# Kernel tuning notes

Measured on AMD Instinct MI355X. Metric: run time of the kernel, lower is better.

The kernel has to match this reference:

```python
import jax, jax.numpy as jnp
import numpy as np


def setup_inputs() -> dict:
    key = jax.random.key(0)
    k1, k2, k3 = jax.random.split(key, 3)
    B, T, D, U = 64, 1024, 256, 256
    inputs = jax.random.normal(k1, (B, T, D), dtype=jnp.float32)
    W_xh = jax.random.normal(k2, (D, U), dtype=jnp.float32) * (1.0 / np.sqrt(D))
    W_hh = jax.random.normal(k3, (U, U), dtype=jnp.float32) * (1.0 / np.sqrt(U))
    b_h = jnp.zeros((U,), dtype=jnp.float32)
    return {"inputs": inputs, "W_xh": W_xh, "W_hh": W_hh, "b_h": b_h}


def reference(inputs, W_xh, W_hh, b_h):
    # inputs: [B, T, D]. Precompute input projection (same math as per-step matmul),
    # then scan the sequential recurrence: h_t = tanh(xW_t + h_{t-1} @ W_hh + b).
    B = inputs.shape[0]
    U = W_hh.shape[0]
    xW = jnp.einsum('btd,du->btu', inputs, W_xh) + b_h  # [B, T, U]
    h0 = jnp.zeros((B, U), dtype=inputs.dtype)

    def step(h, xw_t):
        h_new = jnp.tanh(xw_t + h @ W_hh)
        return h_new, h_new

    _, hs = jax.lax.scan(step, h0, jnp.swapaxes(xW, 0, 1))  # hs: [T, B, U]
    return jnp.swapaxes(hs, 0, 1)  # [B, T, U] (return_sequences=True)
```

## Files before the change

kernel.cpp:

```cpp
#include <hip/hip_runtime.h>
#include <math.h>

#define B_ 64
#define T_ 1024
#define D_ 256
#define U_ 256

typedef __fp16   hf2_t __attribute__((ext_vector_type(2)));
typedef _Float16 f16x8 __attribute__((ext_vector_type(8)));
typedef float    f32x4 __attribute__((ext_vector_type(4)));

__device__ __forceinline__ float fast_tanh2(float x) {
    float e = __expf(2.0f * x);
    return 1.0f - 2.0f * __builtin_amdgcn_rcpf(e + 1.0f);
}

#define CH_  16
#define NCH_ (T_ / CH_)
#define NT2_ 512

__global__ __launch_bounds__(NT2_) __attribute__((amdgpu_waves_per_eu(2, 2)))
void rnn_fused(const float* __restrict__ inputs,
               const float* __restrict__ W_xh,
               const float* __restrict__ W_hh,
               const float* __restrict__ b_h,
               float* __restrict__ out) {
    const int b    = (int)blockIdx.x;
    const int tid  = (int)threadIdx.x;
    const int w    = tid >> 6;
    const int lane = tid & 63;
    const int g    = lane >> 4;
    const int c    = lane & 15;
    const int n0   = w * 32;
    const int cp   = n0 + 2 * c;

    __shared__ __align__(16) _Float16 hl[2][U_];
    __shared__ __align__(16) _Float16 Ax[CH_ * D_];

    f16x8 whh[8][2], wxh[8][2];
    #pragma unroll
    for (int kt = 0; kt < 8; ++kt) {
        #pragma unroll
        for (int nt = 0; nt < 2; ++nt) {
            f16x8 vh, vx;
            #pragma unroll
            for (int j = 0; j < 8; ++j) {
                const int row = kt * 32 + g * 8 + j;
                vh[j] = (_Float16)W_hh[(size_t)row * U_ + cp + nt];
                vx[j] = (_Float16)W_xh[(size_t)row * U_ + cp + nt];
            }
            whh[kt][nt] = vh;
            wxh[kt][nt] = vx;
        }
    }
    const float bb0 = b_h[cp];
    const float bb1 = b_h[cp + 1];

    if (tid < 128) ((float*)&hl[0][0])[tid] = 0.f;

    const float* ibase = inputs + (size_t)b * T_ * D_;
    float* gbase = out + (size_t)b * T_ * U_;

    const int srow = tid >> 5;
    const int sk8  = (tid & 31) * 8;
    char* const sdst = (char*)Ax + srow * 512 + ((sk8 * 2) ^ ((srow & 7) << 4));
    const int vbaseA = c * 512 + ((g * 16) ^ ((c & 7) << 4));

    const f32x4 zero4 = {0.f, 0.f, 0.f, 0.f};

#define PACK8(DST, F0, F1)                                                    \
    {                                                                         \
        union { hf2_t p[4]; f16x8 v; } u;                                     \
        u.p[0] = __builtin_amdgcn_cvt_pkrtz((F0).x, (F0).y);                  \
        u.p[1] = __builtin_amdgcn_cvt_pkrtz((F0).z, (F0).w);                  \
        u.p[2] = __builtin_amdgcn_cvt_pkrtz((F1).x, (F1).y);                  \
        u.p[3] = __builtin_amdgcn_cvt_pkrtz((F1).z, (F1).w);                  \
        *(f16x8*)(DST) = u.v;                                                 \
    }

#define MFMA16(A, BF, ACC) \
    ACC = __builtin_amdgcn_mfma_f32_16x16x32_f16((A), (BF), (ACC), 0, 0, 0)

#define BAR()                                                                 \
    asm volatile("s_waitcnt lgkmcnt(0)" ::: "memory");                        \
    __builtin_amdgcn_s_barrier();                                             \
    asm volatile("" ::: "memory");

    f32x4 qa = zero4, qb = zero4;

#define PROJECT()                                                             \
    {                                                                         \
        f32x4 q0 = zero4, q1 = zero4, q2 = zero4, q3 = zero4;                 \
        _Pragma("unroll") for (int kt = 0; kt < 4; ++kt) {                    \
            f16x8 a = *(const f16x8*)((const char*)Ax + (vbaseA ^ (kt * 64)));\
            MFMA16(a, wxh[kt][0], q0); MFMA16(a, wxh[kt][1], q1);             \
        }                                                                     \
        _Pragma("unroll") for (int kt = 4; kt < 8; ++kt) {                    \
            f16x8 a = *(const f16x8*)((const char*)Ax + (vbaseA ^ (kt * 64)));\
            MFMA16(a, wxh[kt][0], q2); MFMA16(a, wxh[kt][1], q3);             \
        }                                                                     \
        _Pragma("unroll") for (int r = 0; r < 4; ++r) {                       \
            qa[r] = q0[r] + q2[r] + bb0;                                      \
            qb[r] = q1[r] + q3[r] + bb1;                                      \
        }                                                                     \
    }

    {
        float4 f0 = *(const float4*)&ibase[8 * tid];
        float4 f1 = *(const float4*)&ibase[8 * tid + 4];
        PACK8(sdst, f0, f1)
    }
    __syncthreads();
    PROJECT()
    float4 p0, p1;
    {
        const float* gs = ibase + (size_t)CH_ * D_;
        p0 = *(const float4*)&gs[8 * tid];
        p1 = *(const float4*)&gs[8 * tid + 4];
    }
    BAR()

    const char* hrd = (const char*)&hl[0][0] + g * 16;
    char*       hwr = (char*)&hl[0][0] + cp * 2;

#define STEP(J)                                                               \
    {                                                                         \
        const int RD = ((J) & 1) * 512;                                       \
        const int WR = 512 - RD;                                              \
        __builtin_amdgcn_s_setprio(1);                                        \
        f16x8 af0 = *(const f16x8*)(hrd + RD);                                \
        f32x4 ca0 = zero4, ca1 = zero4, cb0 = zero4, cb1 = zero4;             \
        MFMA16(af0, whh[0][0], ca0); MFMA16(af0, whh[0][1], ca1);             \
        _Pragma("unroll") for (int kt = 1; kt < 4; ++kt) {                    \
            f16x8 a = *(const f16x8*)(hrd + RD + 64 * kt);                    \
            MFMA16(a, whh[kt][0], ca0); MFMA16(a, whh[kt][1], ca1);           \
        }                                                                     \
        _Pragma("unroll") for (int kt = 4; kt < 8; ++kt) {                    \
            f16x8 a = *(const f16x8*)(hrd + RD + 64 * kt);                    \
            MFMA16(a, whh[kt][0], cb0); MFMA16(a, whh[kt][1], cb1);           \
        }                                                                     \
        __builtin_amdgcn_s_setprio(0);                                        \
        if (g == ((J) >> 2)) {                                                \
            const float h0 = fast_tanh2(ca0[0] + cb0[0] + qa[(J) & 3]);       \
            const float h1 = fast_tanh2(ca1[0] + cb1[0] + qb[(J) & 3]);       \
            *(hf2_t*)(hwr + WR) = __builtin_amdgcn_cvt_pkrtz(h0, h1);         \
            float* go = gbase + (size_t)(ch * CH_ + (J)) * U_ + cp;           \
            *(float2*)go = make_float2(h0, h1);                               \
        }                                                                     \
        BAR()                                                                 \
    }

    for (int ch = 0; ch < NCH_; ++ch) {
        STEP(0)  STEP(1)  STEP(2)  STEP(3)
        STEP(4)  STEP(5)  STEP(6)  STEP(7)
        STEP(8)  STEP(9)  STEP(10) STEP(11)
        STEP(12) STEP(13) STEP(14) STEP(15)

        if (ch + 1 < NCH_) { PACK8(sdst, p0, p1) }
        BAR()
        if (ch + 1 < NCH_) PROJECT()
        if (ch + 2 < NCH_) {
            const float* gs = ibase + (size_t)(ch + 2) * CH_ * D_;
            p0 = *(const float4*)&gs[8 * tid];
            p1 = *(const float4*)&gs[8 * tid + 4];
        }
    }
#undef STEP
#undef PROJECT
#undef BAR
#undef MFMA16
#undef PACK8
}

extern "C" void kernel_launch(void* const* d_in, const int* in_sizes, int n_in,
                              void* d_out, int out_size, void* d_ws, size_t ws_size,
                              hipStream_t stream) {
    const float* inputs = (const float*)d_in[0];
    const float* W_xh   = (const float*)d_in[1];
    const float* W_hh   = (const float*)d_in[2];
    const float* b_h    = (const float*)d_in[3];
    float* out = (float*)d_out;

    rnn_fused<<<B_, NT2_, 0, stream>>>(inputs, W_xh, W_hh, b_h, out);
}
```

Before: 516.8 us.

## Interleave next-chunk input projection MFMAs into recurrent steps

Removes the separate per-chunk projection phase. The next chunk's input-projection MFMAs are spread across the first 8 recurrent steps, one k-slice per step, and accumulate into qn0/qn1. The input prefetch pipeline is deepened by one chunk, with an extra prologue stage, so the shared staging buffer holds chunk ch+1 while steps of chunk ch run. It also drops the s_setprio hints. The intent is to fill MFMA idle slots in the latency-bound recurrence and shorten the chunk-boundary stall. The cost is extra work on the serial step path for the first 8 steps.

```diff
diff --git a/kernel.cpp b/kernel.cpp
--- a/kernel.cpp
+++ b/kernel.cpp
@@ -87,23 +87,7 @@
     asm volatile("" ::: "memory");
 
     f32x4 qa = zero4, qb = zero4;
-
-#define PROJECT()                                                             \
-    {                                                                         \
-        f32x4 q0 = zero4, q1 = zero4, q2 = zero4, q3 = zero4;                 \
-        _Pragma("unroll") for (int kt = 0; kt < 4; ++kt) {                    \
-            f16x8 a = *(const f16x8*)((const char*)Ax + (vbaseA ^ (kt * 64)));\
-            MFMA16(a, wxh[kt][0], q0); MFMA16(a, wxh[kt][1], q1);             \
-        }                                                                     \
-        _Pragma("unroll") for (int kt = 4; kt < 8; ++kt) {                    \
-            f16x8 a = *(const f16x8*)((const char*)Ax + (vbaseA ^ (kt * 64)));\
-            MFMA16(a, wxh[kt][0], q2); MFMA16(a, wxh[kt][1], q3);             \
-        }                                                                     \
-        _Pragma("unroll") for (int r = 0; r < 4; ++r) {                       \
-            qa[r] = q0[r] + q2[r] + bb0;                                      \
-            qb[r] = q1[r] + q3[r] + bb1;                                      \
-        }                                                                     \
-    }
+    f32x4 qn0 = zero4, qn1 = zero4;
 
     {
         float4 f0 = *(const float4*)&ibase[8 * tid];
@@ -111,14 +95,38 @@
         PACK8(sdst, f0, f1)
     }
     __syncthreads();
-    PROJECT()
+    {
+        f32x4 q0 = zero4, q1 = zero4, q2 = zero4, q3 = zero4;
+        #pragma unroll
+        for (int kt = 0; kt < 4; ++kt) {
+            f16x8 a = *(const f16x8*)((const char*)Ax + (vbaseA ^ (kt * 64)));
+            MFMA16(a, wxh[kt][0], q0); MFMA16(a, wxh[kt][1], q1);
+        }
+        #pragma unroll
+        for (int kt = 4; kt < 8; ++kt) {
+            f16x8 a = *(const f16x8*)((const char*)Ax + (vbaseA ^ (kt * 64)));
+            MFMA16(a, wxh[kt][0], q2); MFMA16(a, wxh[kt][1], q3);
+        }
+        #pragma unroll
+        for (int r = 0; r < 4; ++r) {
+            qa[r] = q0[r] + q2[r] + bb0;
+            qb[r] = q1[r] + q3[r] + bb1;
+        }
+    }
+    BAR()
+    {
+        const float* gs = ibase + (size_t)CH_ * D_;
+        float4 f0 = *(const float4*)&gs[8 * tid];
+        float4 f1 = *(const float4*)&gs[8 * tid + 4];
+        PACK8(sdst, f0, f1)
+    }
+    BAR()
     float4 p0, p1;
     {
-        const float* gs = ibase + (size_t)CH_ * D_;
+        const float* gs = ibase + (size_t)2 * CH_ * D_;
         p0 = *(const float4*)&gs[8 * tid];
         p1 = *(const float4*)&gs[8 * tid + 4];
     }
-    BAR()
 
     const char* hrd = (const char*)&hl[0][0] + g * 16;
     char*       hwr = (char*)&hl[0][0] + cp * 2;
@@ -127,7 +135,6 @@
     {                                                                         \
         const int RD = ((J) & 1) * 512;                                       \
         const int WR = 512 - RD;                                              \
-        __builtin_amdgcn_s_setprio(1);                                        \
         f16x8 af0 = *(const f16x8*)(hrd + RD);                                \
         f32x4 ca0 = zero4, ca1 = zero4, cb0 = zero4, cb1 = zero4;             \
         MFMA16(af0, whh[0][0], ca0); MFMA16(af0, whh[0][1], ca1);             \
@@ -139,7 +146,10 @@
             f16x8 a = *(const f16x8*)(hrd + RD + 64 * kt);                    \
             MFMA16(a, whh[kt][0], cb0); MFMA16(a, whh[kt][1], cb1);           \
         }                                                                     \
-        __builtin_amdgcn_s_setprio(0);                                        \
+        if ((J) < 8) {             \
+            f16x8 ax = *(const f16x8*)((const char*)Ax + (vbaseA ^ ((J)*64)));\
+            MFMA16(ax, wxh[(J)][0], qn0); MFMA16(ax, wxh[(J)][1], qn1);       \
+        }                                                                     \
         if (g == ((J) >> 2)) {                                                \
             const float h0 = fast_tanh2(ca0[0] + cb0[0] + qa[(J) & 3]);       \
             const float h1 = fast_tanh2(ca1[0] + cb1[0] + qb[(J) & 3]);       \
@@ -156,17 +166,21 @@
         STEP(8)  STEP(9)  STEP(10) STEP(11)
         STEP(12) STEP(13) STEP(14) STEP(15)
 
-        if (ch + 1 < NCH_) { PACK8(sdst, p0, p1) }
+        #pragma unroll
+        for (int r = 0; r < 4; ++r) {
+            qa[r] = qn0[r] + bb0;
+            qb[r] = qn1[r] + bb1;
+        }
+        qn0 = zero4; qn1 = zero4;
+        if (ch + 2 < NCH_) { PACK8(sdst, p0, p1) }
         BAR()
-        if (ch + 1 < NCH_) PROJECT()
-        if (ch + 2 < NCH_) {
-            const float* gs = ibase + (size_t)(ch + 2) * CH_ * D_;
+        if (ch + 3 < NCH_) {
+            const float* gs = ibase + (size_t)(ch + 3) * CH_ * D_;
             p0 = *(const float4*)&gs[8 * tid];
             p1 = *(const float4*)&gs[8 * tid + 4];
         }
     }
 #undef STEP
-#undef PROJECT
 #undef BAR
 #undef MFMA16
 #undef PACK8
```

Result: no change. 513.5 us (-0.6%).
